# Optimization experiments

Hardware: AMD Instinct MI355X
Metric: run time of the kernel (lower is better)

The kernel has to match this reference:

```python
import jax, jax.numpy as jnp
import numpy as np

V, F, H, W, K, B, J = 50000, 100000, 256, 256, 1, 4, 256

def setup_inputs() -> dict:
    key = jax.random.key(0)
    ks = jax.random.split(key, 8)
    pix_to_face = jax.random.randint(ks[0], (1, H, W, K), 0, F, dtype=jnp.int32)
    bary = jax.random.uniform(ks[1], (1, H, W, K, 3), dtype=jnp.float32)
    bary = bary / jnp.sum(bary, axis=-1, keepdims=True)  # valid barycentric weights
    faces = jax.random.randint(ks[2], (F, 3), 0, V, dtype=jnp.int32)
    verts = jax.random.normal(ks[3], (V, 3), dtype=jnp.float32)
    vertex_normals = jax.random.normal(ks[4], (V, 3), dtype=jnp.float32)
    directions = jax.random.normal(ks[5], (B, J, 3), dtype=jnp.float32)
    directions = directions / jnp.linalg.norm(directions, axis=-1, keepdims=True)
    env_colors = jax.random.uniform(ks[6], (B, J, 3), dtype=jnp.float32)  # environment_map * sineweight
    texels = jax.random.uniform(ks[7], (1, H, W, 3), dtype=jnp.float32)
    return {"pix_to_face": pix_to_face, "bary_coords": bary, "faces": faces,
            "verts": verts, "vertex_normals": vertex_normals,
            "directions": directions, "env_colors": env_colors, "texels": texels}

def reference(pix_to_face, bary_coords, faces, verts, vertex_normals, directions, env_colors, texels):
    # interpolate_face_attributes: gather per-face vertex normals, bary-weighted sum
    faces_normals = vertex_normals[faces]                     # (F, 3verts, 3)
    attr = faces_normals[pix_to_face]                         # (1, H, W, K, 3verts, 3)
    pixel_normals = jnp.einsum('nhwkv,nhwkvc->nhwkc', bary_coords, attr)[:, :, :, 0, :]  # (1,H,W,3)
    # F.normalize(p=2, dim=-1, eps=1e-6): divide by clamped norm
    norm = jnp.maximum(jnp.linalg.norm(pixel_normals, axis=-1, keepdims=True), 1e-6)
    pixel_normals = pixel_normals / norm
    normals = jnp.broadcast_to(pixel_normals, (directions.shape[0],) + pixel_normals.shape[1:])  # (B,H,W,3)
    # diffuse dot products over all J lights, clamped to [0,1]
    diffuse = jnp.clip(jnp.einsum('bhwc,bjc->bhwj', normals, directions), 0.0, 1.0)  # (B,H,W,J)
    diffuse = jnp.einsum('bjc,bhwj->bhwc', env_colors, diffuse)                      # (B,H,W,3)
    colors = diffuse * texels
    return colors, diffuse, texels, normals
```

## Files before the change

kernel.cpp:

```cpp
#include <hip/hip_runtime.h>

#define NPIX  65536
#define BB    4
#define JJ    256


struct F3 { float x, y, z; };
struct I3 { int x, y, z; };

__global__ __launch_bounds__(256, 8) void shade_kernel(
    const int*   __restrict__ p2f,
    const float* __restrict__ bary,
    const int*   __restrict__ faces,
    const float* __restrict__ vnorm,
    const float* __restrict__ dirs,
    const float* __restrict__ env,
    const float* __restrict__ tex,
    float*       __restrict__ out)
{
    const int b     = blockIdx.x >> 9;
    const int pbase = (blockIdx.x & 511) << 7;
    const int t     = threadIdx.x;
    const int i     = t & 63;
    const int w     = t >> 6;
    const int jh    = __builtin_amdgcn_readfirstlane(w >> 1);
    const int q     = ((w & 1) << 6) | i;

    __shared__ float4 nlds[128];
    __shared__ float  part[128][3];

    const F3* __restrict__ bary3  = (const F3*)bary;
    const I3* __restrict__ faces3 = (const I3*)faces;
    const F3* __restrict__ vn3    = (const F3*)vnorm;
    const F3* __restrict__ tex3   = (const F3*)tex;

    if (jh == 0) {
        const int p = pbase + q;
        const int f = p2f[p];
        const I3 vv = faces3[f];
        const F3 bc = bary3[p];
        const F3 a0 = vn3[vv.x];
        const F3 a1 = vn3[vv.y];
        const F3 a2 = vn3[vv.z];
        float nx = bc.x*a0.x + bc.y*a1.x + bc.z*a2.x;
        float ny = bc.x*a0.y + bc.y*a1.y + bc.z*a2.y;
        float nz = bc.x*a0.z + bc.y*a1.z + bc.z*a2.z;
        const float inv = 1.0f / fmaxf(sqrtf(nx*nx + ny*ny + nz*nz), 1e-6f);
        nx *= inv; ny *= inv; nz *= inv;
        nlds[q] = make_float4(nx, ny, nz, 0.f);

        float* __restrict__ nor = out + (3*BB*NPIX*2 + 3*NPIX);
        const int o = 3*(b*NPIX + p);
        nor[o+0] = nx; nor[o+1] = ny; nor[o+2] = nz;

        if (b == 0) {
            const F3 tv = tex3[p];
            float* __restrict__ tx = out + 3*BB*NPIX*2;
            tx[3*p+0] = tv.x; tx[3*p+1] = tv.y; tx[3*p+2] = tv.z;
        }
    }
    __syncthreads();

    const float4 n = nlds[q];
    float ar = 0.f, ag = 0.f, ab = 0.f;
    const float* __restrict__ dp = dirs + b*(JJ*3) + jh*(128*3);
    const float* __restrict__ ep = env  + b*(JJ*3) + jh*(128*3);

    #pragma unroll 8
    for (int j = 0; j < 128; ++j) {
        const float dx = dp[3*j+0], dy = dp[3*j+1], dz = dp[3*j+2];
        const float er = ep[3*j+0], eg = ep[3*j+1], eb = ep[3*j+2];
        float wgt = fmaf(n.z, dz, fmaf(n.y, dy, n.x*dx));
        wgt = fmaxf(wgt, 0.f);
        ar = fmaf(er, wgt, ar); ag = fmaf(eg, wgt, ag); ab = fmaf(eb, wgt, ab);
    }

    if (jh == 1) {
        part[q][0] = ar; part[q][1] = ag; part[q][2] = ab;
    }
    __syncthreads();

    if (jh == 0) {
        const float sr = ar + part[q][0];
        const float sg = ag + part[q][1];
        const float sb = ab + part[q][2];

        const int p = pbase + q;
        const F3 tv = tex3[p];
        const int o = 3*(b*NPIX + p);
        out[o+0] = sr*tv.x; out[o+1] = sg*tv.y; out[o+2] = sb*tv.z;

        float* __restrict__ dif = out + 3*BB*NPIX;
        dif[o+0] = sr; dif[o+1] = sg; dif[o+2] = sb;
    }
}

extern "C" void kernel_launch(void* const* d_in, const int* in_sizes, int n_in,
                              void* d_out, int out_size, void* d_ws, size_t ws_size,
                              hipStream_t stream) {
    const int*   p2f   = (const int*)  d_in[0];
    const float* bary  = (const float*)d_in[1];
    const int*   faces = (const int*)  d_in[2];
    const float* vnorm = (const float*)d_in[4];
    const float* dirs  = (const float*)d_in[5];
    const float* env   = (const float*)d_in[6];
    const float* tex   = (const float*)d_in[7];
    float* out = (float*)d_out;

    const int grid = BB * (NPIX / 128);
    shade_kernel<<<grid, 256, 0, stream>>>(
        p2f, bary, faces, vnorm, dirs, env, tex, out);
}
```

Baseline: 21.52 us.

## Share per-pixel normal gather across all batches within one block

Blocks now cover 64 pixels across all 4 batch entries: 512 threads arranged as batch by light-half by pixel. Each normal is gathered and normalized once instead of once per batch. This removes the 4x redundant random gathers of faces and vertex normals. Normal and texel stores move to the jh==1 waves, which balances the epilogue, and the loop unroll rises to 16. The grid shrinks to 1024 blocks of 512 threads, so fewer threads do the gather phase and occupancy may change.

```diff
diff --git a/kernel.cpp b/kernel.cpp
--- a/kernel.cpp
+++ b/kernel.cpp
@@ -8,7 +8,7 @@
 struct F3 { float x, y, z; };
 struct I3 { int x, y, z; };
 
-__global__ __launch_bounds__(256, 8) void shade_kernel(
+__global__ __launch_bounds__(512, 8) void shade_kernel(
     const int*   __restrict__ p2f,
     const float* __restrict__ bary,
     const int*   __restrict__ faces,
@@ -18,24 +18,22 @@
     const float* __restrict__ tex,
     float*       __restrict__ out)
 {
-    const int b     = blockIdx.x >> 9;
-    const int pbase = (blockIdx.x & 511) << 7;
+    const int pbase = blockIdx.x << 6;
     const int t     = threadIdx.x;
-    const int i     = t & 63;
-    const int w     = t >> 6;
-    const int jh    = __builtin_amdgcn_readfirstlane(w >> 1);
-    const int q     = ((w & 1) << 6) | i;
+    const int L     = t & 63;
+    const int b     = __builtin_amdgcn_readfirstlane(t >> 7);
+    const int jh    = __builtin_amdgcn_readfirstlane((t >> 6) & 1);
 
-    __shared__ float4 nlds[128];
-    __shared__ float  part[128][3];
+    __shared__ float4 nlds[64];
+    __shared__ float4 part[4][64];
 
     const F3* __restrict__ bary3  = (const F3*)bary;
     const I3* __restrict__ faces3 = (const I3*)faces;
     const F3* __restrict__ vn3    = (const F3*)vnorm;
     const F3* __restrict__ tex3   = (const F3*)tex;
 
-    if (jh == 0) {
-        const int p = pbase + q;
+    if (t < 64) {
+        const int p = pbase + t;
         const int f = p2f[p];
         const I3 vv = faces3[f];
         const F3 bc = bary3[p];
@@ -47,11 +45,31 @@
         float nz = bc.x*a0.z + bc.y*a1.z + bc.z*a2.z;
         const float inv = 1.0f / fmaxf(sqrtf(nx*nx + ny*ny + nz*nz), 1e-6f);
         nx *= inv; ny *= inv; nz *= inv;
-        nlds[q] = make_float4(nx, ny, nz, 0.f);
+        nlds[t] = make_float4(nx, ny, nz, 0.f);
+    }
+    __syncthreads();
 
+    const float4 n = nlds[L];
+    float ar = 0.f, ag = 0.f, ab = 0.f;
+    const float* __restrict__ dp = dirs + b*(JJ*3) + jh*(128*3);
+    const float* __restrict__ ep = env  + b*(JJ*3) + jh*(128*3);
+
+    #pragma unroll 16
+    for (int j = 0; j < 128; ++j) {
+        const float dx = dp[3*j+0], dy = dp[3*j+1], dz = dp[3*j+2];
+        const float er = ep[3*j+0], eg = ep[3*j+1], eb = ep[3*j+2];
+        float wgt = fmaf(n.z, dz, fmaf(n.y, dy, n.x*dx));
+        wgt = fmaxf(wgt, 0.f);
+        ar = fmaf(er, wgt, ar); ag = fmaf(eg, wgt, ag); ab = fmaf(eb, wgt, ab);
+    }
+
+    if (jh == 1) {
+        part[b][L] = make_float4(ar, ag, ab, 0.f);
+
+        const int p = pbase + L;
         float* __restrict__ nor = out + (3*BB*NPIX*2 + 3*NPIX);
         const int o = 3*(b*NPIX + p);
-        nor[o+0] = nx; nor[o+1] = ny; nor[o+2] = nz;
+        nor[o+0] = n.x; nor[o+1] = n.y; nor[o+2] = n.z;
 
         if (b == 0) {
             const F3 tv = tex3[p];
@@ -61,31 +79,13 @@
     }
     __syncthreads();
 
-    const float4 n = nlds[q];
-    float ar = 0.f, ag = 0.f, ab = 0.f;
-    const float* __restrict__ dp = dirs + b*(JJ*3) + jh*(128*3);
-    const float* __restrict__ ep = env  + b*(JJ*3) + jh*(128*3);
+    if (jh == 0) {
+        const float4 q = part[b][L];
+        const float sr = ar + q.x;
+        const float sg = ag + q.y;
+        const float sb = ab + q.z;
 
-    #pragma unroll 8
-    for (int j = 0; j < 128; ++j) {
-        const float dx = dp[3*j+0], dy = dp[3*j+1], dz = dp[3*j+2];
-        const float er = ep[3*j+0], eg = ep[3*j+1], eb = ep[3*j+2];
-        float wgt = fmaf(n.z, dz, fmaf(n.y, dy, n.x*dx));
-        wgt = fmaxf(wgt, 0.f);
-        ar = fmaf(er, wgt, ar); ag = fmaf(eg, wgt, ag); ab = fmaf(eb, wgt, ab);
-    }
-
-    if (jh == 1) {
-        part[q][0] = ar; part[q][1] = ag; part[q][2] = ab;
-    }
-    __syncthreads();
-
-    if (jh == 0) {
-        const float sr = ar + part[q][0];
-        const float sg = ag + part[q][1];
-        const float sb = ab + part[q][2];
-
-        const int p = pbase + q;
+        const int p = pbase + L;
         const F3 tv = tex3[p];
         const int o = 3*(b*NPIX + p);
         out[o+0] = sr*tv.x; out[o+1] = sg*tv.y; out[o+2] = sb*tv.z;
@@ -107,7 +107,7 @@
     const float* tex   = (const float*)d_in[7];
     float* out = (float*)d_out;
 
-    const int grid = BB * (NPIX / 128);
-    shade_kernel<<<grid, 256, 0, stream>>>(
+    const int grid = NPIX / 64;
+    shade_kernel<<<grid, 512, 0, stream>>>(
         p2f, bary, faces, vnorm, dirs, env, tex, out);
 }
```

After: 19.96 us. 1.08x faster.

## Split lights across four waves with packed float2 math over two pixels

Applied to the files above, without the earlier changes.

Each wave now takes a quarter of the lights and handles two pixels per lane using packed two-wide float FMA/max operations, so the instruction stream can map onto the packed FP32 VALU ops. Directions and environment colours are read as float4 chunks to cut scalar load count. The four partial sums are reduced through shared memory. Launch bounds occupancy hint is lowered, trading occupancy for register headroom.

```diff
diff --git a/kernel.cpp b/kernel.cpp
--- a/kernel.cpp
+++ b/kernel.cpp
@@ -7,8 +7,9 @@
 
 struct F3 { float x, y, z; };
 struct I3 { int x, y, z; };
+typedef float f2 __attribute__((ext_vector_type(2)));
 
-__global__ __launch_bounds__(256, 8) void shade_kernel(
+__global__ __launch_bounds__(256, 4) void shade_kernel(
     const int*   __restrict__ p2f,
     const float* __restrict__ bary,
     const int*   __restrict__ faces,
@@ -23,19 +24,18 @@
     const int t     = threadIdx.x;
     const int i     = t & 63;
     const int w     = t >> 6;
-    const int jh    = __builtin_amdgcn_readfirstlane(w >> 1);
-    const int q     = ((w & 1) << 6) | i;
+    const int jq    = __builtin_amdgcn_readfirstlane(w);
 
     __shared__ float4 nlds[128];
-    __shared__ float  part[128][3];
+    __shared__ f2     part[4][64][3];
 
     const F3* __restrict__ bary3  = (const F3*)bary;
     const I3* __restrict__ faces3 = (const I3*)faces;
     const F3* __restrict__ vn3    = (const F3*)vnorm;
     const F3* __restrict__ tex3   = (const F3*)tex;
 
-    if (jh == 0) {
-        const int p = pbase + q;
+    if (t < 128) {
+        const int p = pbase + t;
         const int f = p2f[p];
         const I3 vv = faces3[f];
         const F3 bc = bary3[p];
@@ -47,7 +47,7 @@
         float nz = bc.x*a0.z + bc.y*a1.z + bc.z*a2.z;
         const float inv = 1.0f / fmaxf(sqrtf(nx*nx + ny*ny + nz*nz), 1e-6f);
         nx *= inv; ny *= inv; nz *= inv;
-        nlds[q] = make_float4(nx, ny, nz, 0.f);
+        nlds[t] = make_float4(nx, ny, nz, 0.f);
 
         float* __restrict__ nor = out + (3*BB*NPIX*2 + 3*NPIX);
         const int o = 3*(b*NPIX + p);
@@ -61,31 +61,56 @@
     }
     __syncthreads();
 
-    const float4 n = nlds[q];
-    float ar = 0.f, ag = 0.f, ab = 0.f;
-    const float* __restrict__ dp = dirs + b*(JJ*3) + jh*(128*3);
-    const float* __restrict__ ep = env  + b*(JJ*3) + jh*(128*3);
+    const float4 nA = nlds[i];
+    const float4 nB = nlds[64 + i];
+    const f2 nx2 = {nA.x, nB.x};
+    const f2 ny2 = {nA.y, nB.y};
+    const f2 nz2 = {nA.z, nB.z};
+    f2 ar2 = {0.f, 0.f}, ag2 = {0.f, 0.f}, ab2 = {0.f, 0.f};
 
-    #pragma unroll 8
-    for (int j = 0; j < 128; ++j) {
-        const float dx = dp[3*j+0], dy = dp[3*j+1], dz = dp[3*j+2];
-        const float er = ep[3*j+0], eg = ep[3*j+1], eb = ep[3*j+2];
-        float wgt = fmaf(n.z, dz, fmaf(n.y, dy, n.x*dx));
-        wgt = fmaxf(wgt, 0.f);
-        ar = fmaf(er, wgt, ar); ag = fmaf(eg, wgt, ag); ab = fmaf(eb, wgt, ab);
+    const float4* __restrict__ d4 = (const float4*)(dirs + (b*JJ + jq*64)*3);
+    const float4* __restrict__ e4 = (const float4*)(env  + (b*JJ + jq*64)*3);
+
+#define LIGHT1(dx,dy,dz,er,eg,eb) {                                     \
+    f2 wv = nx2 * (f2){dx, dx};                                         \
+    wv = __builtin_elementwise_fma(ny2, (f2){dy, dy}, wv);              \
+    wv = __builtin_elementwise_fma(nz2, (f2){dz, dz}, wv);              \
+    wv = __builtin_elementwise_max(wv, (f2){0.f, 0.f});     \
+    ar2 = __builtin_elementwise_fma((f2){er, er}, wv, ar2);             \
+    ag2 = __builtin_elementwise_fma((f2){eg, eg}, wv, ag2);             \
+    ab2 = __builtin_elementwise_fma((f2){eb, eb}, wv, ab2); }
+
+    #pragma unroll 4
+    for (int ch = 0; ch < 16; ++ch) {
+        const float4 D0 = d4[ch*3 + 0];
+        const float4 D1 = d4[ch*3 + 1];
+        const float4 D2 = d4[ch*3 + 2];
+        const float4 E0 = e4[ch*3 + 0];
+        const float4 E1 = e4[ch*3 + 1];
+        const float4 E2 = e4[ch*3 + 2];
+        LIGHT1(D0.x, D0.y, D0.z,  E0.x, E0.y, E0.z)
+        LIGHT1(D0.w, D1.x, D1.y,  E0.w, E1.x, E1.y)
+        LIGHT1(D1.z, D1.w, D2.x,  E1.z, E1.w, E2.x)
+        LIGHT1(D2.y, D2.z, D2.w,  E2.y, E2.z, E2.w)
     }
+#undef LIGHT1
 
-    if (jh == 1) {
-        part[q][0] = ar; part[q][1] = ag; part[q][2] = ab;
-    }
+    part[w][i][0] = ar2;
+    part[w][i][1] = ag2;
+    part[w][i][2] = ab2;
     __syncthreads();
 
-    if (jh == 0) {
-        const float sr = ar + part[q][0];
-        const float sg = ag + part[q][1];
-        const float sb = ab + part[q][2];
+    if (t < 128) {
+        const int ls = t & 63;
+        const int e  = t >> 6;
+        const float sr = part[0][ls][0][e] + part[1][ls][0][e]
+                       + part[2][ls][0][e] + part[3][ls][0][e];
+        const float sg = part[0][ls][1][e] + part[1][ls][1][e]
+                       + part[2][ls][1][e] + part[3][ls][1][e];
+        const float sb = part[0][ls][2][e] + part[1][ls][2][e]
+                       + part[2][ls][2][e] + part[3][ls][2][e];
 
-        const int p = pbase + q;
+        const int p = pbase + (e << 6) + ls;
         const F3 tv = tex3[p];
         const int o = 3*(b*NPIX + p);
         out[o+0] = sr*tv.x; out[o+1] = sg*tv.y; out[o+2] = sb*tv.z;
```

Measured after the change: 18.63 us. -13.4%, faster.
